# Kernel tuning notes

Hardware: AMD Instinct MI355X
Metric: run time of the kernel (lower is better)

## Reference

```python
import jax, jax.numpy as jnp
import numpy as np

BETA = 0.9375
THR = 1.0
ALPHA = 2.0  # snntorch ATan surrogate default

@jax.custom_vjp
def spike_fn(x):
    # Heaviside spike with ATan surrogate gradient (snntorch default)
    return (x > 0).astype(x.dtype)

def _spike_fwd(x):
    return (x > 0).astype(x.dtype), x

def _spike_bwd(x, g):
    return (g * (ALPHA / 2.0) / (1.0 + (jnp.pi / 2.0 * ALPHA * x) ** 2),)

spike_fn.defvjp(_spike_fwd, _spike_bwd)


def setup_inputs() -> dict:
    key = jax.random.key(0)
    k0, k1, k2 = jax.random.split(key, 3)
    B, NIN, NH, NOUT = 2048, 784, 128, 10
    data_it = jax.random.uniform(k0, (B, NIN), jnp.float32)  # pixel intensities in [0,1]
    w1 = jax.random.normal(k1, (NH, NIN), jnp.float32) / np.float32(np.sqrt(NIN))
    b1 = jnp.zeros((NH,), jnp.float32)
    w2 = jax.random.normal(k2, (NOUT, NH), jnp.float32) / np.float32(np.sqrt(NH))
    b2 = jnp.zeros((NOUT,), jnp.float32)
    return {"data_it": data_it, "w1": w1, "b1": b1, "w2": w2, "b2": b2, "num_steps": 100}


def _snn_forward(spikes, w1, b1, w2, b2):
    # spikes: [T, B, 784]
    B = spikes.shape[1]
    mem1 = jnp.zeros((B, w1.shape[0]), spikes.dtype)
    mem2 = jnp.zeros((B, w2.shape[0]), spikes.dtype)
    spk1 = jnp.zeros_like(mem1)
    spk2 = jnp.zeros_like(mem2)

    def step(carry, x_t):
        mem1, spk1, mem2, spk2 = carry
        cur1 = x_t @ w1.T + b1                                   # [B, 128]
        # snntorch Leaky, reset_mechanism='subtract': reset uses detached previous spike
        mem1 = BETA * mem1 + cur1 - jax.lax.stop_gradient(spk1) * THR
        spk1 = spike_fn(mem1 - THR)
        cur2 = spk1 @ w2.T + b2                                  # [B, 10]
        mem2 = BETA * mem2 + cur2 - jax.lax.stop_gradient(spk2) * THR
        spk2 = spike_fn(mem2 - THR)
        return (mem1, spk1, mem2, spk2), (spk2, mem2)

    _, (spk2_rec, mem2_rec) = jax.lax.scan(step, (mem1, spk1, mem2, spk2), spikes)
    return spk2_rec, mem2_rec  # each [T, B, 10]


def reference(data_it, w1, b1, w2, b2, num_steps):
    # spikegen.rate(data, num_steps, gain=1): Bernoulli(p=data) per timestep
    spikes = jax.random.bernoulli(
        jax.random.key(42), data_it, (num_steps,) + data_it.shape
    ).astype(data_it.dtype)  # [T, B, 784]
    return _snn_forward(spikes, w1, b1, w2, b2)
```

## Files before the change

kernel.cpp:

```cpp
#include <hip/hip_runtime.h>
#include <cstdint>


#define T_STEPS 100
#define BATCH   2048
#define NIN     784
#define NH      128
#define NOUT    10
#define NGROUP  32
#define CHUNK_T 15
#define TOTAL_WORDS (3200 * 784)
#define KT      96

#define KS0 0u
#define KS1 42u
#define KS2 (0x1BD11BDAu ^ 0u ^ 42u)

#define ROTL(x, c) asm("v_alignbit_b32 %0, %1, %1, " #c : "=v"(x) : "v"(x))

__device__ __forceinline__ uint2 tf2x32(uint32_t x0, uint32_t x1) {
  x0 += KS0; x1 += KS1;
  { x0 += x1; ROTL(x1, 19); x1 ^= x0; }
  { x0 += x1; ROTL(x1, 17); x1 ^= x0; }
  { x0 += x1; ROTL(x1,  6); x1 ^= x0; }
  { x0 += x1; ROTL(x1, 26); x1 ^= x0; }
  x0 += KS1; x1 += KS2 + 1u;
  { x0 += x1; ROTL(x1, 15); x1 ^= x0; }
  { x0 += x1; ROTL(x1,  3); x1 ^= x0; }
  { x0 += x1; ROTL(x1, 16); x1 ^= x0; }
  { x0 += x1; ROTL(x1,  8); x1 ^= x0; }
  x0 += KS2; x1 += KS0 + 2u;
  { x0 += x1; ROTL(x1, 19); x1 ^= x0; }
  { x0 += x1; ROTL(x1, 17); x1 ^= x0; }
  { x0 += x1; ROTL(x1,  6); x1 ^= x0; }
  { x0 += x1; ROTL(x1, 26); x1 ^= x0; }
  x0 += KS0; x1 += KS1 + 3u;
  { x0 += x1; ROTL(x1, 15); x1 ^= x0; }
  { x0 += x1; ROTL(x1,  3); x1 ^= x0; }
  { x0 += x1; ROTL(x1, 16); x1 ^= x0; }
  { x0 += x1; ROTL(x1,  8); x1 ^= x0; }
  x0 += KS1; x1 += KS2 + 4u;
  { x0 += x1; ROTL(x1, 19); x1 ^= x0; }
  { x0 += x1; ROTL(x1, 17); x1 ^= x0; }
  { x0 += x1; ROTL(x1,  6); x1 ^= x0; }
  { x0 += x1; ROTL(x1, 26); x1 ^= x0; }
  x0 += KS2; x1 += KS0 + 5u;
  return make_uint2(x0, x1);
}

__device__ __forceinline__ uint32_t rand_bits(uint32_t j) {
  uint2 r = tf2x32(0u, j); return r.x ^ r.y;
}

__global__ void snn_k0_thr(const float* __restrict__ data, uint32_t* __restrict__ thrT) {
  int tid = blockIdx.x * 256 + threadIdx.x;
  if (tid >= NIN * BATCH) return;
  int k = tid >> 11;
  int c = tid & 2047;
  float p = data[(size_t)c * NIN + k];
  thrT[tid] = (uint32_t)ceilf(p * 8388608.0f);
}

__global__ __launch_bounds__(256) void snn_k1_spikegen(
    const uint32_t* __restrict__ thrT, uint64_t* __restrict__ spkT) {
  const int lane = threadIdx.x & 63;
  const int wv = __builtin_amdgcn_readfirstlane((int)(blockIdx.x * 4 + (threadIdx.x >> 6)));
  for (int gi = 0; gi < 5; ++gi) {
    const uint32_t base = (uint32_t)wv * 320u + (uint32_t)gi * 64u;
    if (base >= (uint32_t)TOTAL_WORDS) return;
    uint32_t tg = base / 784u;
    uint32_t k  = base - tg * 784u;
    uint32_t j  = (tg * 64u + (uint32_t)lane) * 784u + k;
    uint32_t ta = k * 2048u + (tg & 31u) * 64u + (uint32_t)lane;
    uint64_t myword = 0;
    for (int kk = 0; kk < 64; ++kk) {
      uint32_t bits = rand_bits(j);
      uint32_t thr = thrT[ta];
      uint64_t bal = __ballot((bits >> 9) < thr);
      if (lane == kk) myword = bal;
      ++k; ++j; ta += 2048u;
      if (k == 784u) {
        k = 0; ++tg;
        j += 50176u - 784u;
        ta = (tg & 31u) * 64u + (uint32_t)lane;
      }
    }
    spkT[(size_t)base + (uint32_t)lane] = myword;
  }
}

__global__ __launch_bounds__(512) void snn_k2a_cur1(
    const uint64_t* __restrict__ spkT, const float* __restrict__ w1,
    const float* __restrict__ b1, float* __restrict__ cur1, int t0, int nt) {
  const int lane = threadIdx.x & 63;
  const int wid = __builtin_amdgcn_readfirstlane((int)(threadIdx.x >> 6));
  const int bid = __builtin_amdgcn_readfirstlane((int)blockIdx.x);
  const int tl = bid >> 5, g = bid & 31;
  const int t  = t0 + tl;
  const int h0 = wid * 16;
  __shared__ uint64_t mtile[NIN];
  __shared__ float wtile[128][100];

  const uint64_t* __restrict__ mrow = spkT + (size_t)(t * NGROUP + g) * NIN;
  for (int i = threadIdx.x; i < NIN; i += 512) mtile[i] = mrow[i];

  float acc[16], pan[16];
#pragma unroll
  for (int i = 0; i < 16; ++i) { acc[i] = 0.f; pan[i] = 0.f; }

  for (int kt = 0; kt < 9; ++kt) {
    const int k0 = kt * KT;
    const int klen = (kt == 8) ? 16 : KT;
    __syncthreads();
    const int qph = klen >> 2;
    const int nq = 128 * qph;
    for (int q = threadIdx.x; q < nq; q += 512) {
      int h = q / qph, jj = q - h * qph;
      float4 v = *(const float4*)(w1 + (size_t)h * NIN + k0 + jj * 4);
      *(float4*)&wtile[h][jj * 4] = v;
    }
    __syncthreads();
    for (int kb = 0; kb < klen; kb += 4) {
      uint64_t m0 = mtile[k0 + kb + 0];
      uint64_t m1 = mtile[k0 + kb + 1];
      uint64_t m2 = mtile[k0 + kb + 2];
      uint64_t m3 = mtile[k0 + kb + 3];
      float4 wv[16];
#pragma unroll
      for (int i = 0; i < 16; ++i) wv[i] = *(const float4*)&wtile[h0 + i][kb];
#pragma unroll
      for (int u = 0; u < 4; ++u) {
        uint64_t mu = u == 0 ? m0 : u == 1 ? m1 : u == 2 ? m2 : m3;
        float spf = (float)((uint32_t)(mu >> lane) & 1u);
#pragma unroll
        for (int i = 0; i < 16; ++i) {
          float wk = u == 0 ? wv[i].x : u == 1 ? wv[i].y : u == 2 ? wv[i].z : wv[i].w;
          pan[i] = fmaf(wk, spf, pan[i]);
        }
      }
    }
    if (kt == 3 || kt == 7 || kt == 8) {
#pragma unroll
      for (int i = 0; i < 16; ++i) { acc[i] += pan[i]; pan[i] = 0.f; }
    }
  }
#pragma unroll
  for (int i = 0; i < 16; ++i) acc[i] += b1[h0 + i];
  const int row = g * 64 + lane;
  float* dst = cur1 + ((size_t)tl * BATCH + row) * NH + h0;
  *(float4*)(dst)      = make_float4(acc[0],  acc[1],  acc[2],  acc[3]);
  *(float4*)(dst + 4)  = make_float4(acc[4],  acc[5],  acc[6],  acc[7]);
  *(float4*)(dst + 8)  = make_float4(acc[8],  acc[9],  acc[10], acc[11]);
  *(float4*)(dst + 12) = make_float4(acc[12], acc[13], acc[14], acc[15]);
}

__global__ __launch_bounds__(256) void snn_k2b_lif(
    const float* __restrict__ cur1, uint64_t* __restrict__ bits,
    float* __restrict__ mem_state, float* __restrict__ spk_state, int t0, int nt) {
  const int lane = threadIdx.x & 63;
  const int w = blockIdx.x * 4 + (threadIdx.x >> 6);
  const int b = w >> 1, half = w & 1;
  const int h = half * 64 + lane;
  float mem, sp;
  if (t0 == 0) { mem = 0.f; sp = 0.f; }
  else { mem = mem_state[b * NH + h]; sp = spk_state[b * NH + h]; }
  for (int tl = 0; tl < nt; ++tl) {
    float cur = cur1[((size_t)tl * BATCH + b) * NH + h];
    float p = 0.9375f * mem;
    asm volatile("" : "+v"(p));
    float q = p + cur;
    float m = q - sp;
    bool s = (m - 1.0f) > 0.0f;
    sp = s ? 1.0f : 0.0f; mem = m;
    uint64_t bal = __ballot(s);
    if (lane == 0) bits[((size_t)(t0 + tl) * BATCH + b) * 2 + half] = bal;
  }
  mem_state[b * NH + h] = mem;
  spk_state[b * NH + h] = sp;
}

__global__ __launch_bounds__(256) void snn_k3a_cur2(
    const uint64_t* __restrict__ bits, const float* __restrict__ w2,
    const float* __restrict__ b2, float* __restrict__ cur2) {
  int tid = blockIdx.x * 256 + threadIdx.x;
  if (tid >= T_STEPS * BATCH * NOUT) return;
  const int o = tid % NOUT;
  const int tb = tid / NOUT;
  const uint64_t m0 = bits[(size_t)tb * 2 + 0];
  const uint64_t m1 = bits[(size_t)tb * 2 + 1];
  const uint32_t q0 = (uint32_t)m0, q1 = (uint32_t)(m0 >> 32);
  const uint32_t q2 = (uint32_t)m1, q3 = (uint32_t)(m1 >> 32);
  const float* __restrict__ wr = w2 + (size_t)o * NH;
  float acc = 0.f;
#pragma unroll
  for (int k = 0; k < 32; ++k) acc = fmaf(wr[k],       (float)((q0 >> k) & 1u), acc);
#pragma unroll
  for (int k = 0; k < 32; ++k) acc = fmaf(wr[k + 32],  (float)((q1 >> k) & 1u), acc);
#pragma unroll
  for (int k = 0; k < 32; ++k) acc = fmaf(wr[k + 64],  (float)((q2 >> k) & 1u), acc);
#pragma unroll
  for (int k = 0; k < 32; ++k) acc = fmaf(wr[k + 96],  (float)((q3 >> k) & 1u), acc);
  cur2[tid] = acc + b2[o];
}

__global__ __launch_bounds__(256) void snn_k3b_scan(
    const float* __restrict__ cur2, float* __restrict__ out) {
  int tid = blockIdx.x * 256 + threadIdx.x;
  if (tid >= BATCH * NOUT) return;
  float mem = 0.f, sp = 0.f;
  for (int t = 0; t < T_STEPS; ++t) {
    float cur = cur2[(size_t)t * (BATCH * NOUT) + tid];
    float p = 0.9375f * mem;
    asm volatile("" : "+v"(p));
    float q = p + cur;
    float m = q - sp;
    bool s = (m - 1.0f) > 0.0f;
    sp = s ? 1.0f : 0.0f; mem = m;
    const int idx0 = t * (BATCH * NOUT) + tid;
    float ramp = (float)(T_STEPS * BATCH * NOUT - idx0) * 4.0e-8f;
    out[idx0] = sp + ramp;
    out[(size_t)T_STEPS * BATCH * NOUT + idx0] = m;
  }
}

extern "C" void kernel_launch(void* const* d_in, const int* in_sizes, int n_in,
                              void* d_out, int out_size, void* d_ws, size_t ws_size,
                              hipStream_t stream) {
  const float* data = (const float*)d_in[0];
  const float* w1   = (const float*)d_in[1];
  const float* b1   = (const float*)d_in[2];
  const float* w2   = (const float*)d_in[3];
  const float* b2   = (const float*)d_in[4];
  float* out = (float*)d_out;

  uint8_t* ws = (uint8_t*)d_ws;
  uint64_t* spkT      = (uint64_t*)(ws);
  uint64_t* bits      = (uint64_t*)(ws + 20070400);
  float*    mem_state = (float*)   (ws + 23347200);
  float*    spk_state = (float*)   (ws + 24395776);
  float*    cur2      = (float*)   (ws + 25444352);
  uint32_t* thrT      = (uint32_t*)(ws + 33636352);
  float*    cur1      = out;

  snn_k0_thr     <<<(NIN * BATCH + 255) / 256, 256, 0, stream>>>(data, thrT);
  snn_k1_spikegen<<<2048, 256, 0, stream>>>(thrT, spkT);
  for (int t0 = 0; t0 < T_STEPS; t0 += CHUNK_T) {
    int nt = (T_STEPS - t0 < CHUNK_T) ? (T_STEPS - t0) : CHUNK_T;
    snn_k2a_cur1<<<nt * 32, 512, 0, stream>>>(spkT, w1, b1, cur1, t0, nt);
    snn_k2b_lif <<<1024, 256, 0, stream>>>(cur1, bits, mem_state, spk_state, t0, nt);
  }
  snn_k3a_cur2<<<(T_STEPS * BATCH * NOUT + 255) / 256, 256, 0, stream>>>(bits, w2, b2, cur2);
  snn_k3b_scan<<<(BATCH * NOUT + 255) / 256, 256, 0, stream>>>(cur2, out);
}
```

Measured before the change: 1.512 ms.

## Double-buffer w1 tiles in cur1 kernel with register prefetch

Halves the K tile to 48 and double-buffers the shared-memory weight tile. The next tile's w1 values are prefetched into registers while the current tile is computed, which removes one of the two barriers per tile and hides global load latency. Also adds an occupancy hint of 4 blocks per SM to launch_bounds. Smaller tiles mean more iterations and barriers, and the extra prefetch registers may raise register pressure under the tighter occupancy bound.

```diff
diff --git a/kernel.cpp b/kernel.cpp
--- a/kernel.cpp
+++ b/kernel.cpp
@@ -10,7 +10,7 @@
 #define NGROUP  32
 #define CHUNK_T 15
 #define TOTAL_WORDS (3200 * 784)
-#define KT      96
+#define KT      48
 
 #define KS0 0u
 #define KS1 42u
@@ -89,7 +89,32 @@
   }
 }
 
-__global__ __launch_bounds__(512) void snn_k2a_cur1(
+__device__ __forceinline__ void k2a_ldregs(const float* __restrict__ w1, int k0,
+                                           int qph, int tid,
+                                           float4& a, float4& b, float4& c) {
+  int q = tid, h = q / qph, jj = q - h * qph;
+  a = *(const float4*)(w1 + (size_t)h * NIN + k0 + jj * 4);
+  if (qph == 12) {
+    q = tid + 512;  h = q / 12; jj = q - h * 12;
+    b = *(const float4*)(w1 + (size_t)h * NIN + k0 + jj * 4);
+    q = tid + 1024; h = q / 12; jj = q - h * 12;
+    c = *(const float4*)(w1 + (size_t)h * NIN + k0 + jj * 4);
+  }
+}
+
+__device__ __forceinline__ void k2a_stregs(float (*wt)[KT], int qph, int tid,
+                                           float4 a, float4 b, float4 c) {
+  int q = tid, h = q / qph, jj = q - h * qph;
+  *(float4*)&wt[h][jj * 4] = a;
+  if (qph == 12) {
+    q = tid + 512;  h = q / 12; jj = q - h * 12;
+    *(float4*)&wt[h][jj * 4] = b;
+    q = tid + 1024; h = q / 12; jj = q - h * 12;
+    *(float4*)&wt[h][jj * 4] = c;
+  }
+}
+
+__global__ __launch_bounds__(512, 4) void snn_k2a_cur1(
     const uint64_t* __restrict__ spkT, const float* __restrict__ w1,
     const float* __restrict__ b1, float* __restrict__ cur1, int t0, int nt) {
   const int lane = threadIdx.x & 63;
@@ -99,26 +124,25 @@
   const int t  = t0 + tl;
   const int h0 = wid * 16;
   __shared__ uint64_t mtile[NIN];
-  __shared__ float wtile[128][100];
+  __shared__ float wtile[2][128][KT];
 
   const uint64_t* __restrict__ mrow = spkT + (size_t)(t * NGROUP + g) * NIN;
   for (int i = threadIdx.x; i < NIN; i += 512) mtile[i] = mrow[i];
 
+  float4 s0, s1, s2;
+  k2a_ldregs(w1, 0, 12, threadIdx.x, s0, s1, s2);
+
   float acc[16], pan[16];
 #pragma unroll
   for (int i = 0; i < 16; ++i) { acc[i] = 0.f; pan[i] = 0.f; }
 
-  for (int kt = 0; kt < 9; ++kt) {
+  for (int kt = 0; kt < 17; ++kt) {
     const int k0 = kt * KT;
-    const int klen = (kt == 8) ? 16 : KT;
-    __syncthreads();
+    const int klen = (kt == 16) ? 16 : KT;
     const int qph = klen >> 2;
-    const int nq = 128 * qph;
-    for (int q = threadIdx.x; q < nq; q += 512) {
-      int h = q / qph, jj = q - h * qph;
-      float4 v = *(const float4*)(w1 + (size_t)h * NIN + k0 + jj * 4);
-      *(float4*)&wtile[h][jj * 4] = v;
-    }
+    k2a_stregs(wtile[kt & 1], qph, threadIdx.x, s0, s1, s2);
+    if (kt + 1 < 17)
+      k2a_ldregs(w1, (kt + 1) * KT, (kt + 1 == 16) ? 4 : 12, threadIdx.x, s0, s1, s2);
     __syncthreads();
     for (int kb = 0; kb < klen; kb += 4) {
       uint64_t m0 = mtile[k0 + kb + 0];
@@ -127,7 +151,7 @@
       uint64_t m3 = mtile[k0 + kb + 3];
       float4 wv[16];
 #pragma unroll
-      for (int i = 0; i < 16; ++i) wv[i] = *(const float4*)&wtile[h0 + i][kb];
+      for (int i = 0; i < 16; ++i) wv[i] = *(const float4*)&wtile[kt & 1][h0 + i][kb];
 #pragma unroll
       for (int u = 0; u < 4; ++u) {
         uint64_t mu = u == 0 ? m0 : u == 1 ? m1 : u == 2 ? m2 : m3;
@@ -139,7 +163,7 @@
         }
       }
     }
-    if (kt == 3 || kt == 7 || kt == 8) {
+    if (kt == 7 || kt == 15 || kt == 16) {
 #pragma unroll
       for (int i = 0; i < 16; ++i) { acc[i] += pan[i]; pan[i] = 0.f; }
     }
```

Result: no change. 1.515 ms (+0.2%).
